# Kernel optimization log

Measured on AMD Instinct MI355X. Metric: run time of the kernel, lower is better.

Reference implementation:

```python
import jax, jax.numpy as jnp
import numpy as np

FEAT_STRIDE = 16
NEG_THR, POS_THR = 0.3, 0.7        # cfg.TRAIN.RPN_NEGATIVE_OVERLAP / RPN_POSITIVE_OVERLAP
RPN_BATCHSIZE, NUM_FG = 256, 128   # RPN_BATCHSIZE, FG_FRACTION=0.5
A_PER_LOC = 9


def generate_anchors(base_size=16, ratios=(0.5, 1.0, 2.0), scales=(8, 16, 32)):
    w = h = float(base_size)
    xc = yc = 0.5 * (base_size - 1)
    size = w * h
    ws = np.round(np.sqrt(size / np.array(ratios)))
    hs = np.round(ws * np.array(ratios))
    out = []
    for wi, hi in zip(ws, hs):
        for s in scales:
            W, H = wi * s, hi * s
            out.append([xc - 0.5 * (W - 1), yc - 0.5 * (H - 1),
                        xc + 0.5 * (W - 1), yc + 0.5 * (H - 1)])
    return np.array(out, dtype=np.float32)  # [9, 4]


def _forward(rpn_cls_score, gt_boxes, im_info):
    B, _, H, W = rpn_cls_score.shape
    A = A_PER_LOC
    base = jnp.asarray(generate_anchors())
    sx, sy = jnp.meshgrid(jnp.arange(W) * FEAT_STRIDE, jnp.arange(H) * FEAT_STRIDE)  # 'xy', [H,W]
    shifts = jnp.stack([sx.ravel(), sy.ravel(), sx.ravel(), sy.ravel()], 1).astype(jnp.float32)  # [K,4]
    anchors = (base[None, :, :] + shifts[:, None, :]).reshape(-1, 4)  # [N=K*A, 4], (h,w,a)-major
    N = anchors.shape[0]

    img_h, img_w = im_info[0, 0], im_info[0, 1]
    inside = ((anchors[:, 0] >= 0) & (anchors[:, 1] >= 0) &
              (anchors[:, 2] < img_w) & (anchors[:, 3] < img_h))  # [N]

    # ---- IoU overlaps (torch +1 pixel convention) ----
    gt = gt_boxes[..., :4]  # [B,Kg,4]
    aw = anchors[:, 2] - anchors[:, 0] + 1.0
    ah = anchors[:, 3] - anchors[:, 1] + 1.0
    a_area = aw * ah                                   # [N]
    g_area = (gt[..., 2] - gt[..., 0] + 1.0) * (gt[..., 3] - gt[..., 1] + 1.0)  # [B,Kg]
    ix = jnp.maximum(0.0, jnp.minimum(anchors[None, :, None, 2], gt[:, None, :, 2])
                     - jnp.maximum(anchors[None, :, None, 0], gt[:, None, :, 0]) + 1.0)
    iy = jnp.maximum(0.0, jnp.minimum(anchors[None, :, None, 3], gt[:, None, :, 3])
                     - jnp.maximum(anchors[None, :, None, 1], gt[:, None, :, 1]) + 1.0)
    inter = ix * iy
    ovr = inter / (a_area[None, :, None] + g_area[:, None, :] - inter)  # [B,N,Kg]

    max_ovr = ovr.max(2)
    arg = ovr.argmax(2)                                 # [B,N]
    ovr_in = jnp.where(inside[None, :, None], ovr, 0.0)  # only in-image anchors compete for gt-max
    gt_max = ovr_in.max(1)                              # [B,Kg]
    gt_max = jnp.where(gt_max == 0.0, 1e-5, gt_max)
    is_best = (ovr_in == gt_max[:, None, :]).any(2)     # [B,N]

    # ---- label assignment (RPN_CLOBBER_POSITIVES = False) ----
    lbl = jnp.full((B, N), -1.0, jnp.float32)
    lbl = jnp.where(inside[None] & (max_ovr < NEG_THR), 0.0, lbl)
    lbl = jnp.where(inside[None] & is_best, 1.0, lbl)
    lbl = jnp.where(inside[None] & (max_ovr >= POS_THR), 1.0, lbl)

    # ---- random fg/bg subsampling (deterministic jax PRNG replaces np.random.permutation) ----
    def _subsample(lbl_b, key):
        kf, kb = jax.random.split(key)
        def disable(l, mask, limit, k):
            prio = jnp.where(mask, jax.random.uniform(k, l.shape), -1.0)
            order = jnp.argsort(-prio)
            rank = jnp.zeros(l.shape[0], jnp.int32).at[order].set(jnp.arange(l.shape[0], dtype=jnp.int32))
            return jnp.where(mask & (rank >= limit), -1.0, l)
        lbl_b = disable(lbl_b, lbl_b == 1.0, NUM_FG, kf)
        num_bg = RPN_BATCHSIZE - jnp.sum(lbl_b == 1.0)
        return disable(lbl_b, lbl_b == 0.0, num_bg, kb)

    lbl = jax.vmap(_subsample)(lbl, jax.random.split(jax.random.key(42), B))

    assigned = jnp.take_along_axis(gt, arg[..., None], axis=1)  # [B,N,4]
    acx = anchors[:, 0] + 0.5 * (aw - 1.0)
    acy = anchors[:, 1] + 0.5 * (ah - 1.0)
    g_w = assigned[..., 2] - assigned[..., 0] + 1.0
    g_h = assigned[..., 3] - assigned[..., 1] + 1.0
    gcx = assigned[..., 0] + 0.5 * (g_w - 1.0)
    gcy = assigned[..., 1] + 0.5 * (g_h - 1.0)
    targets = jnp.stack([(gcx - acx[None]) / aw[None], (gcy - acy[None]) / ah[None],
                         jnp.log(g_w / aw[None]), jnp.log(g_h / ah[None])], -1)  # [B,N,4]

    in_w = jnp.where(lbl == 1.0, 1.0, 0.0)             # RPN_BBOX_INSIDE_WEIGHTS = 1
    num_examples = jnp.sum(lbl >= 0.0, axis=1).astype(jnp.float32)  # RPN_POSITIVE_WEIGHT = -1
    uw = 1.0 / num_examples                             # uniform pos/neg weight, per batch
    out_w = jnp.where((lbl == 1.0) | (lbl == 0.0), uw[:, None], 0.0)

    # ---- _unmap with fill=0 for out-of-image anchors ----
    lbl = jnp.where(inside[None], lbl, 0.0)
    targets = jnp.where(inside[None, :, None], targets, 0.0)
    in_w = jnp.where(inside[None], in_w, 0.0)
    out_w = jnp.where(inside[None], out_w, 0.0)

    labels_out = lbl.reshape(B, H, W, A).transpose(0, 3, 1, 2).reshape(B, 1, A * H, W)
    targets_out = targets.reshape(B, H, W, 4 * A).transpose(0, 3, 1, 2)
    in_w_out = jnp.broadcast_to(in_w[..., None], (B, N, 4)).reshape(B, H, W, 4 * A).transpose(0, 3, 1, 2)
    out_w_out = jnp.broadcast_to(out_w[..., None], (B, N, 4)).reshape(B, H, W, 4 * A).transpose(0, 3, 1, 2)
    return labels_out, targets_out, in_w_out, out_w_out


def setup_inputs() -> dict:
    key = jax.random.key(0)
    B, A, H, W, Kg = 16, 9, 64, 64, 50
    k1, k2, k3, k4, k5 = jax.random.split(key, 5)
    rpn_cls_score = jax.random.normal(k1, (B, 2 * A, H, W), jnp.float32)
    # valid GT boxes inside a 1024x1024 image, class label in column 4
    x1 = jax.random.uniform(k2, (B, Kg)) * 800.0
    y1 = jax.random.uniform(k3, (B, Kg)) * 800.0
    w = 20.0 + jax.random.uniform(k4, (B, Kg)) * 200.0
    h = 20.0 + jax.random.uniform(k5, (B, Kg)) * 200.0
    cls = jnp.ones((B, Kg), jnp.float32)
    gt_boxes = jnp.stack([x1, y1, x1 + w, y1 + h, cls], -1)
    im_info = jnp.full((B, 2), 1024.0, jnp.float32)
    return {"rpn_cls_score": rpn_cls_score, "gt_boxes": gt_boxes, "im_info": im_info, "num_boxes": Kg}


def reference(rpn_cls_score, gt_boxes, im_info, num_boxes):
    return _forward(rpn_cls_score, gt_boxes, im_info)
```

## Files before the change

### kernel.cpp

```cpp
#include <hip/hip_runtime.h>
#include <stdint.h>


#define B_   16
#define A_   9
#define H_   64
#define W_   64
#define HW_  (H_*W_)
#define N_   (HW_*A_)
#define KG_  50
#define S0_  (B_*A_*HW_)
#define S1_  (B_*4*A_*HW_)
#define NGTB_ (B_*KG_)
#define LCLR_ ((B_*N_ + NGTB_ - 1) / NGTB_)

typedef unsigned long long ull;

__constant__ float c_base[A_][4] = {
  { -84.f,  -40.f,  99.f,  55.f},
  {-176.f,  -88.f, 191.f, 103.f},
  {-360.f, -184.f, 375.f, 199.f},
  { -56.f,  -56.f,  71.f,  71.f},
  {-120.f, -120.f, 135.f, 135.f},
  {-248.f, -248.f, 263.f, 263.f},
  { -36.f,  -80.f,  51.f,  95.f},
  { -80.f, -168.f,  95.f, 183.f},
  {-168.f, -344.f, 183.f, 359.f},
};

__device__ __forceinline__ void tf2x32(uint32_t k0, uint32_t k1,
                                       uint32_t x0, uint32_t x1,
                                       uint32_t& o0, uint32_t& o1) {
  const uint32_t ks2 = k0 ^ k1 ^ 0x1BD11BDAu;
  uint32_t ks[3] = {k0, k1, ks2};
  x0 += ks[0]; x1 += ks[1];
  const int R[2][4] = {{13,15,26,6},{17,29,16,24}};
  #pragma unroll
  for (int i = 0; i < 5; i++) {
    #pragma unroll
    for (int j = 0; j < 4; j++) {
      x0 += x1;
      int r = R[i & 1][j];
      x1 = (x1 << r) | (x1 >> (32 - r));
      x1 ^= x0;
    }
    x0 += ks[(i + 1) % 3];
    x1 += ks[(i + 2) % 3] + (uint32_t)(i + 1);
  }
  o0 = x0; o1 = x1;
}

__device__ __attribute__((noinline))
float box_area_f(float x1, float y1, float x2, float y2) {
#pragma clang fp contract(off)
  return (x2 - x1 + 1.f) * (y2 - y1 + 1.f);
}

__device__ __attribute__((noinline))
float iou_core(float ax1, float ay1, float ax2, float ay2, float aarea,
               float gx1, float gy1, float gx2, float gy2, float garea) {
#pragma clang fp contract(off)
  float ix = fmaxf(fminf(ax2, gx2) - fmaxf(ax1, gx1) + 1.f, 0.f);
  float iy = fmaxf(fminf(ay2, gy2) - fmaxf(ay1, gy1) + 1.f, 0.f);
  float inter = ix * iy;
  return inter / (aarea + garea - inter);
}

__global__ __launch_bounds__(256) void k_gtmax(const float* __restrict__ gtb,
                                               const float* __restrict__ iminfo,
                                               float* __restrict__ gt_max,
                                               uint32_t* __restrict__ keys,
                                               float* __restrict__ lbl) {
  const int b = blockIdx.x / KG_;
  const int g = blockIdx.x % KG_;
  const int tid = threadIdx.x;
  if (blockIdx.x == 0 && tid < B_) {
    uint32_t k0, k1, kf0, kf1, kb0, kb1;
    tf2x32(0u, 42u, 0u, (uint32_t)tid, k0, k1);
    tf2x32(k0, k1, 0u, 0u, kf0, kf1);
    tf2x32(k0, k1, 0u, 1u, kb0, kb1);
    keys[tid * 4 + 0] = kf0;
    keys[tid * 4 + 1] = kf1;
    keys[tid * 4 + 2] = kb0;
    keys[tid * 4 + 3] = kb1;
  }
  {
    const int base = blockIdx.x * LCLR_;
    const int lim = min(base + LCLR_, B_ * N_);
    for (int i = base + tid; i < lim; i += 256) lbl[i] = -1.f;
  }
  const float* gp = gtb + (b * KG_ + g) * 5;
  const float gx1 = gp[0], gy1 = gp[1], gx2 = gp[2], gy2 = gp[3];
  const float garea = box_area_f(gx1, gy1, gx2, gy2);
  const float imh = iminfo[0], imw = iminfo[1];
  float best = 0.f;
  for (int a = 0; a < A_; a++) {
    const float bx1 = c_base[a][0], by1 = c_base[a][1];
    const float bx2 = c_base[a][2], by2 = c_base[a][3];
    const float aarea = box_area_f(bx1, by1, bx2, by2);
    int xlo = max(0, (int)ceilf(-bx1 / 16.f));
    int xhi = min(W_ - 1, (int)ceilf((imw - bx2) / 16.f) - 1);
    int ylo = max(0, (int)ceilf(-by1 / 16.f));
    int yhi = min(H_ - 1, (int)ceilf((imh - by2) / 16.f) - 1);
    xlo = max(xlo, (int)floorf((gx1 - 1.f - bx2) / 16.f));
    xhi = min(xhi, (int)ceilf((gx2 + 1.f - bx1) / 16.f));
    ylo = max(ylo, (int)floorf((gy1 - 1.f - by2) / 16.f));
    yhi = min(yhi, (int)ceilf((gy2 + 1.f - by1) / 16.f));
    const int nx = xhi - xlo + 1, ny = yhi - ylo + 1;
    if (nx <= 0 || ny <= 0) continue;
    const int lw = (nx <= 1) ? 0 : (32 - __clz(nx - 1));
    const int tot = ny << lw;
    const int mask = (1 << lw) - 1;
    for (int t = tid; t < tot; t += 256) {
      const int xi = t & mask;
      if (xi >= nx) continue;
      const int x = xlo + xi;
      const int y = ylo + (t >> lw);
      const float sx = 16.f * (float)x, sy = 16.f * (float)y;
      best = fmaxf(best, iou_core(bx1 + sx, by1 + sy, bx2 + sx, by2 + sy,
                                  aarea, gx1, gy1, gx2, gy2, garea));
    }
  }
  best = fmaxf(best, __shfl_xor(best, 32));
  best = fmaxf(best, __shfl_xor(best, 16));
  best = fmaxf(best, __shfl_xor(best, 8));
  best = fmaxf(best, __shfl_xor(best, 4));
  best = fmaxf(best, __shfl_xor(best, 2));
  best = fmaxf(best, __shfl_xor(best, 1));
  __shared__ float sw[4];
  if ((tid & 63) == 0) sw[tid >> 6] = best;
  __syncthreads();
  if (tid == 0)
    gt_max[b * KG_ + g] = fmaxf(fmaxf(sw[0], sw[1]), fmaxf(sw[2], sw[3]));
}

__global__ __launch_bounds__(256) void k_fuse(const float* __restrict__ gtb,
                                              const float* __restrict__ iminfo,
                                              const float* __restrict__ gt_max,
                                              const uint32_t* __restrict__ keys,
                                              float* __restrict__ lbl,
                                              int* __restrict__ amax,
                                              uint32_t* __restrict__ priof,
                                              uint32_t* __restrict__ priob) {
  __shared__ float sgx1[KG_], sgy1[KG_], sgx2[KG_], sgy2[KG_], sga[KG_], sgm[KG_];
  __shared__ int s_xlo[A_], s_ylo[A_], s_nx[A_], s_pre[A_ + 1];
  __shared__ uint32_t s_k[4];
  const int b = blockIdx.y;
  const int tid = threadIdx.x;
  if (tid < KG_) {
    const float* g = gtb + (b * KG_ + tid) * 5;
    float x1 = g[0], y1 = g[1], x2 = g[2], y2 = g[3];
    sgx1[tid] = x1; sgy1[tid] = y1; sgx2[tid] = x2; sgy2[tid] = y2;
    sga[tid] = box_area_f(x1, y1, x2, y2);
    float gm = gt_max[b * KG_ + tid];
    sgm[tid] = (gm == 0.f) ? 1e-5f : gm;
  }
  if (tid < 4) s_k[tid] = keys[b * 4 + tid];
  if (tid < A_) {
    const float imh = iminfo[0], imw = iminfo[1];
    const float bx1 = c_base[tid][0], by1 = c_base[tid][1];
    const float bx2 = c_base[tid][2], by2 = c_base[tid][3];
    int xlo = max(0, (int)ceilf(-bx1 / 16.f));
    int xhi = min(W_ - 1, (int)ceilf((imw - bx2) / 16.f) - 1);
    int ylo = max(0, (int)ceilf(-by1 / 16.f));
    int yhi = min(H_ - 1, (int)ceilf((imh - by2) / 16.f) - 1);
    int nx = max(0, xhi - xlo + 1), ny = max(0, yhi - ylo + 1);
    s_xlo[tid] = xlo; s_ylo[tid] = ylo; s_nx[tid] = nx;
    s_pre[tid + 1] = nx * ny;
  }
  __syncthreads();
  if (tid == 0) {
    s_pre[0] = 0;
    for (int a = 0; a < A_; a++) s_pre[a + 1] += s_pre[a];
  }
  __syncthreads();
  const int C = s_pre[A_];

  for (int t = blockIdx.x * 256 + tid; t < C; t += gridDim.x * 256) {
    int a = 0;
    while (t >= s_pre[a + 1]) a++;
    const int idx = t - s_pre[a];
    const int nx = s_nx[a];
    const int y = s_ylo[a] + idx / nx;
    const int x = s_xlo[a] + (idx - (idx / nx) * nx);
    const int n = (y * W_ + x) * A_ + a;
    const float sx = 16.f * (float)x, sy = 16.f * (float)y;
    const float ax1 = c_base[a][0] + sx, ay1 = c_base[a][1] + sy;
    const float ax2 = c_base[a][2] + sx, ay2 = c_base[a][3] + sy;
    const float aarea = box_area_f(c_base[a][0], c_base[a][1],
                                   c_base[a][2], c_base[a][3]);
    float mo = -1.f;
    int bidx = 0;
    bool best = false;
    for (int k = 0; k < KG_; k++) {
      float ovr = iou_core(ax1, ay1, ax2, ay2, aarea,
                           sgx1[k], sgy1[k], sgx2[k], sgy2[k], sga[k]);
      if (ovr > mo) { mo = ovr; bidx = k; }
      best = best || (ovr == sgm[k]);
    }
    float l = -1.f;
    if (mo < 0.3f) l = 0.f;
    if (best || mo >= 0.7f) l = 1.f;
    lbl[(size_t)b * N_ + n] = l;
    amax[(size_t)b * N_ + n] = bidx;
    uint32_t y0, y1;
    tf2x32(s_k[0], s_k[1], 0u, (uint32_t)n, y0, y1);
    priof[(size_t)b * N_ + n] = (y0 ^ y1) >> 9;
    tf2x32(s_k[2], s_k[3], 0u, (uint32_t)n, y0, y1);
    priob[(size_t)b * N_ + n] = (y0 ^ y1) >> 9;
  }
}

__global__ __launch_bounds__(1024) void k_sub3(float* __restrict__ lbl,
                                               const uint32_t* __restrict__ priof,
                                               const uint32_t* __restrict__ priob,
                                               float* __restrict__ uw) {
  const int b = blockIdx.x;
  const int tid = threadIdx.x;
  __shared__ int hf[256], hb[256];
  __shared__ int s_binF, s_rF, s_binB, s_rB, s_needF, s_needB, s_nf, s_nb;
  __shared__ float s_uw;
  __shared__ ull kF[2048], kB[2048];
  __shared__ ull s_KF, s_KB;

  float* L = lbl + (size_t)b * N_;
  const float4* L4 = (const float4*)L;
  const uint4* Pf4 = (const uint4*)(priof + (size_t)b * N_);
  const uint4* Pb4 = (const uint4*)(priob + (size_t)b * N_);

  if (tid < 256) { hf[tid] = 0; hb[tid] = 0; }
  if (tid == 0) { s_nf = 0; s_nb = 0; }
  __syncthreads();

  for (int i4 = tid; i4 < N_ / 4; i4 += 1024) {
    float4 v = L4[i4];
    uint4 mf = Pf4[i4];
    uint4 mb = Pb4[i4];
    const float lv[4] = {v.x, v.y, v.z, v.w};
    const uint32_t fv[4] = {mf.x, mf.y, mf.z, mf.w};
    const uint32_t bv[4] = {mb.x, mb.y, mb.z, mb.w};
    #pragma unroll
    for (int j = 0; j < 4; j++) {
      if (lv[j] == 1.f) atomicAdd(&hf[fv[j] >> 15], 1);
      else if (lv[j] == 0.f) atomicAdd(&hb[bv[j] >> 15], 1);
    }
  }
  __syncthreads();

  if (tid == 0) {
    int acc = 0, binF = -1, rF = 0;
    for (int bin = 255; bin >= 0; bin--) {
      int hv = hf[bin];
      if (binF < 0 && acc + hv >= 128) { binF = bin; rF = 128 - acc; }
      acc += hv;
    }
    const int Mf = acc;
    const int kf = (Mf < 128) ? Mf : 128;
    const int limB = 256 - kf;
    int accb = 0, binB = -1, rB = 0;
    for (int bin = 255; bin >= 0; bin--) {
      int hv = hb[bin];
      if (binB < 0 && accb + hv >= limB) { binB = bin; rB = limB - accb; }
      accb += hv;
    }
    const int Mb = accb;
    const int kb = (Mb < limB) ? Mb : limB;
    s_needF = (Mf > 128);
    s_binF = binF; s_rF = rF;
    s_needB = (Mb > limB);
    s_binB = binB; s_rB = rB;
    s_uw = 1.f / (float)(kf + kb);
  }
  __syncthreads();
  const int needF = s_needF, needB = s_needB;
  const int binF = s_binF, binB = s_binB;

  if (needF || needB) {
    for (int i4 = tid; i4 < N_ / 4; i4 += 1024) {
      float4 v = L4[i4];
      uint4 mf = Pf4[i4];
      uint4 mb = Pb4[i4];
      const float lv[4] = {v.x, v.y, v.z, v.w};
      const uint32_t fv[4] = {mf.x, mf.y, mf.z, mf.w};
      const uint32_t bv[4] = {mb.x, mb.y, mb.z, mb.w};
      #pragma unroll
      for (int j = 0; j < 4; j++) {
        if (needF && lv[j] == 1.f && (int)(fv[j] >> 15) == binF) {
          int p = atomicAdd(&s_nf, 1);
          if (p < 2048)
            kF[p] = ((ull)fv[j] << 16) | (ull)(65535 - (i4 * 4 + j));
        }
        if (needB && lv[j] == 0.f && (int)(bv[j] >> 15) == binB) {
          int p = atomicAdd(&s_nb, 1);
          if (p < 2048)
            kB[p] = ((ull)bv[j] << 16) | (ull)(65535 - (i4 * 4 + j));
        }
      }
    }
    __syncthreads();
    const int sf = min(s_nf, 2048), sb = min(s_nb, 2048);
    if (needF) {
      for (int j = tid; j < sf; j += 1024) {
        ull kj = kF[j];
        int rank = 0;
        for (int q = 0; q < sf; q++) rank += (kF[q] > kj) ? 1 : 0;
        if (rank == s_rF - 1) s_KF = kj;
      }
    }
    if (needB) {
      for (int j = tid; j < sb; j += 1024) {
        ull kj = kB[j];
        int rank = 0;
        for (int q = 0; q < sb; q++) rank += (kB[q] > kj) ? 1 : 0;
        if (rank == s_rB - 1) s_KB = kj;
      }
    }
    __syncthreads();
    const ull KF_ = needF ? s_KF : 0ull;
    const ull KB_ = needB ? s_KB : 0ull;
    for (int i4 = tid; i4 < N_ / 4; i4 += 1024) {
      float4 v = L4[i4];
      uint4 mf = Pf4[i4];
      uint4 mb = Pb4[i4];
      const float lv[4] = {v.x, v.y, v.z, v.w};
      const uint32_t fv[4] = {mf.x, mf.y, mf.z, mf.w};
      const uint32_t bv[4] = {mb.x, mb.y, mb.z, mb.w};
      #pragma unroll
      for (int j = 0; j < 4; j++) {
        if (needF && lv[j] == 1.f) {
          ull key = ((ull)fv[j] << 16) | (ull)(65535 - (i4 * 4 + j));
          if (key < KF_) L[i4 * 4 + j] = -1.f;
        } else if (needB && lv[j] == 0.f) {
          ull key = ((ull)bv[j] << 16) | (ull)(65535 - (i4 * 4 + j));
          if (key < KB_) L[i4 * 4 + j] = -1.f;
        }
      }
    }
  }
  if (tid == 0) uw[b] = s_uw;
}

__global__ __launch_bounds__(256) void k_out(const float* __restrict__ gtb,
                                             const float* __restrict__ iminfo,
                                             const float* __restrict__ lbl,
                                             const int* __restrict__ amax,
                                             const float* __restrict__ uw,
                                             float* __restrict__ out) {
  const int t = blockIdx.x * 256 + threadIdx.x;
  const int w = t & 63;
  const int h = (t >> 6) & 63;
  const int a = (t >> 12) % A_;
  const int b = t / (A_ * HW_);
  const int n = (h * W_ + w) * A_ + a;

  const float ax1 = c_base[a][0] + 16.f * (float)w;
  const float ay1 = c_base[a][1] + 16.f * (float)h;
  const float ax2 = c_base[a][2] + 16.f * (float)w;
  const float ay2 = c_base[a][3] + 16.f * (float)h;
  const float imh = iminfo[0], imw = iminfo[1];
  const bool ins = (ax1 >= 0.f) && (ay1 >= 0.f) && (ax2 < imw) && (ay2 < imh);

  const float l = lbl[(size_t)b * N_ + n];

  out[(size_t)b * (A_ * HW_) + a * HW_ + h * W_ + w] = ins ? l : 0.f;

  float tx = 0.f, ty = 0.f, tw = 0.f, th = 0.f;
  if (ins) {
    const int g = amax[(size_t)b * N_ + n];
    const float* gp = gtb + ((size_t)b * KG_ + g) * 5;
    float aw = ax2 - ax1 + 1.f, ah = ay2 - ay1 + 1.f;
    float acx = ax1 + 0.5f * (aw - 1.f), acy = ay1 + 0.5f * (ah - 1.f);
    float gw = gp[2] - gp[0] + 1.f, gh = gp[3] - gp[1] + 1.f;
    float gcx = gp[0] + 0.5f * (gw - 1.f), gcy = gp[1] + 0.5f * (gh - 1.f);
    tx = (gcx - acx) / aw;
    ty = (gcy - acy) / ah;
    tw = logf(gw / aw);
    th = logf(gh / ah);
  }
  float* o1 = out + S0_;
  const size_t toff = (size_t)b * (4 * A_ * HW_) + (4 * a) * HW_ + h * W_ + w;
  o1[toff]           = tx;
  o1[toff + HW_]     = ty;
  o1[toff + 2 * HW_] = tw;
  o1[toff + 3 * HW_] = th;

  const float inw = (ins && l == 1.f) ? 1.f : 0.f;
  const float oww = (ins && (l == 0.f || l == 1.f)) ? uw[b] : 0.f;
  float* o2 = out + S0_ + S1_;
  o2[toff] = inw; o2[toff + HW_] = inw; o2[toff + 2 * HW_] = inw; o2[toff + 3 * HW_] = inw;
  float* o3 = out + S0_ + 2 * (size_t)S1_;
  o3[toff] = oww; o3[toff + HW_] = oww; o3[toff + 2 * HW_] = oww; o3[toff + 3 * HW_] = oww;
}

extern "C" void kernel_launch(void* const* d_in, const int* in_sizes, int n_in,
                              void* d_out, int out_size, void* d_ws, size_t ws_size,
                              hipStream_t stream) {
  const float* gtb = (const float*)d_in[1];
  const float* iminfo = (const float*)d_in[2];
  float* out = (float*)d_out;

  float* lbl = (float*)d_ws;
  int* amax = (int*)(lbl + (size_t)B_ * N_);
  float* gt_max = (float*)(amax + (size_t)B_ * N_);
  float* uw = gt_max + B_ * KG_;
  uint32_t* keys = (uint32_t*)(uw + B_);
  uint32_t* priof = keys + B_ * 4;
  uint32_t* priob = priof + (size_t)B_ * N_;

  k_gtmax<<<NGTB_, 256, 0, stream>>>(gtb, iminfo, gt_max, keys, lbl);
  k_fuse<<<dim3(73, B_), 256, 0, stream>>>(gtb, iminfo, gt_max, keys,
                                           lbl, amax, priof, priob);
  k_sub3<<<B_, 1024, 0, stream>>>(lbl, priof, priob, uw);
  k_out<<<S0_ / 256, 256, 0, stream>>>(gtb, iminfo, lbl, amax, uw, out);
}
```

Measured before the change: 156.2 us.

## Compact fg/bg candidates and select threshold in parallel per batch-polarity

Instead of writing per-anchor priorities for all anchors and having one 1024-thread block per batch scan labels three times, the fused IoU kernel now compacts labeled anchors into per-batch fg/bg candidate lists and builds global histograms with atomics. A new small select kernel (one block per batch and polarity) finds the k-th largest key from the candidates. The final output kernel recomputes the threefry priority and applies the threshold inline, so the full -1 label clear and the priority buffers go away. This trades the serial per-batch scans for global atomics, a fixed candidate capacity (which could overflow if labeled counts exceed it), and duplicated RNG work in the output kernel.

```diff
diff --git a/kernel.cpp b/kernel.cpp
--- a/kernel.cpp
+++ b/kernel.cpp
@@ -12,7 +12,8 @@
 #define S0_  (B_*A_*HW_)
 #define S1_  (B_*4*A_*HW_)
 #define NGTB_ (B_*KG_)
-#define LCLR_ ((B_*N_ + NGTB_ - 1) / NGTB_)
+#define CAP_  20480
+#define NHIST_ (B_*2*256 + B_*2)
 
 typedef unsigned long long ull;
 
@@ -70,7 +71,7 @@
                                                const float* __restrict__ iminfo,
                                                float* __restrict__ gt_max,
                                                uint32_t* __restrict__ keys,
-                                               float* __restrict__ lbl) {
+                                               int* __restrict__ cnt_hist) {
   const int b = blockIdx.x / KG_;
   const int g = blockIdx.x % KG_;
   const int tid = threadIdx.x;
@@ -84,10 +85,11 @@
     keys[tid * 4 + 2] = kb0;
     keys[tid * 4 + 3] = kb1;
   }
-  {
-    const int base = blockIdx.x * LCLR_;
-    const int lim = min(base + LCLR_, B_ * N_);
-    for (int i = base + tid; i < lim; i += 256) lbl[i] = -1.f;
+  if (blockIdx.x < 32) {
+    const int per = (NHIST_ + 31) / 32;
+    const int base = blockIdx.x * per;
+    const int lim = min(base + per, NHIST_);
+    for (int i = base + tid; i < lim; i += 256) cnt_hist[i] = 0;
   }
   const float* gp = gtb + (b * KG_ + g) * 5;
   const float gx1 = gp[0], gy1 = gp[1], gx2 = gp[2], gy2 = gp[3];
@@ -140,11 +142,13 @@
                                               const uint32_t* __restrict__ keys,
                                               float* __restrict__ lbl,
                                               int* __restrict__ amax,
-                                              uint32_t* __restrict__ priof,
-                                              uint32_t* __restrict__ priob) {
+                                              ull* __restrict__ cand,
+                                              int* __restrict__ cnt,
+                                              int* __restrict__ hist) {
   __shared__ float sgx1[KG_], sgy1[KG_], sgx2[KG_], sgy2[KG_], sga[KG_], sgm[KG_];
   __shared__ int s_xlo[A_], s_ylo[A_], s_nx[A_], s_pre[A_ + 1];
   __shared__ uint32_t s_k[4];
+  __shared__ int s_num[2], s_base[2];
   const int b = blockIdx.y;
   const int tid = threadIdx.x;
   if (tid < KG_) {
@@ -156,6 +160,7 @@
     sgm[tid] = (gm == 0.f) ? 1e-5f : gm;
   }
   if (tid < 4) s_k[tid] = keys[b * 4 + tid];
+  if (tid < 2) s_num[tid] = 0;
   if (tid < A_) {
     const float imh = iminfo[0], imw = iminfo[1];
     const float bx1 = c_base[tid][0], by1 = c_base[tid][1];
@@ -175,15 +180,19 @@
   }
   __syncthreads();
   const int C = s_pre[A_];
-
-  for (int t = blockIdx.x * 256 + tid; t < C; t += gridDim.x * 256) {
+  const int t = blockIdx.x * 256 + tid;
+
+  bool act = false;
+  int p = 0, lpos = 0, n = 0;
+  uint32_t m = 0;
+  if (t < C) {
     int a = 0;
     while (t >= s_pre[a + 1]) a++;
     const int idx = t - s_pre[a];
     const int nx = s_nx[a];
     const int y = s_ylo[a] + idx / nx;
     const int x = s_xlo[a] + (idx - (idx / nx) * nx);
-    const int n = (y * W_ + x) * A_ + a;
+    n = (y * W_ + x) * A_ + a;
     const float sx = 16.f * (float)x, sy = 16.f * (float)y;
     const float ax1 = c_base[a][0] + sx, ay1 = c_base[a][1] + sy;
     const float ax2 = c_base[a][2] + sx, ay2 = c_base[a][3] + sy;
@@ -203,148 +212,85 @@
     if (best || mo >= 0.7f) l = 1.f;
     lbl[(size_t)b * N_ + n] = l;
     amax[(size_t)b * N_ + n] = bidx;
-    uint32_t y0, y1;
-    tf2x32(s_k[0], s_k[1], 0u, (uint32_t)n, y0, y1);
-    priof[(size_t)b * N_ + n] = (y0 ^ y1) >> 9;
-    tf2x32(s_k[2], s_k[3], 0u, (uint32_t)n, y0, y1);
-    priob[(size_t)b * N_ + n] = (y0 ^ y1) >> 9;
-  }
-}
-
-__global__ __launch_bounds__(1024) void k_sub3(float* __restrict__ lbl,
-                                               const uint32_t* __restrict__ priof,
-                                               const uint32_t* __restrict__ priob,
-                                               float* __restrict__ uw) {
-  const int b = blockIdx.x;
+    if (l >= 0.f) {
+      act = true;
+      p = (l == 1.f) ? 0 : 1;
+      uint32_t y0, y1;
+      tf2x32(s_k[2 * p], s_k[2 * p + 1], 0u, (uint32_t)n, y0, y1);
+      m = (y0 ^ y1) >> 9;
+      lpos = atomicAdd(&s_num[p], 1);
+    }
+  }
+  __syncthreads();
+  if (tid < 2 && s_num[tid] > 0)
+    s_base[tid] = atomicAdd(&cnt[b * 2 + tid], s_num[tid]);
+  __syncthreads();
+  if (act) {
+    cand[(size_t)(b * 2 + p) * CAP_ + s_base[p] + lpos] =
+        ((ull)m << 16) | (ull)(65535 - n);
+    atomicAdd(&hist[(b * 2 + p) * 256 + (int)(m >> 15)], 1);
+  }
+}
+
+__global__ __launch_bounds__(256) void k_select(const ull* __restrict__ cand,
+                                                const int* __restrict__ cnt,
+                                                const int* __restrict__ hist,
+                                                ull* __restrict__ Kstar,
+                                                float* __restrict__ uw) {
+  const int b = blockIdx.x >> 1, p = blockIdx.x & 1;
   const int tid = threadIdx.x;
-  __shared__ int hf[256], hb[256];
-  __shared__ int s_binF, s_rF, s_binB, s_rB, s_needF, s_needB, s_nf, s_nb;
-  __shared__ float s_uw;
-  __shared__ ull kF[2048], kB[2048];
-  __shared__ ull s_KF, s_KB;
-
-  float* L = lbl + (size_t)b * N_;
-  const float4* L4 = (const float4*)L;
-  const uint4* Pf4 = (const uint4*)(priof + (size_t)b * N_);
-  const uint4* Pb4 = (const uint4*)(priob + (size_t)b * N_);
-
-  if (tid < 256) { hf[tid] = 0; hb[tid] = 0; }
-  if (tid == 0) { s_nf = 0; s_nb = 0; }
-  __syncthreads();
-
-  for (int i4 = tid; i4 < N_ / 4; i4 += 1024) {
-    float4 v = L4[i4];
-    uint4 mf = Pf4[i4];
-    uint4 mb = Pb4[i4];
-    const float lv[4] = {v.x, v.y, v.z, v.w};
-    const uint32_t fv[4] = {mf.x, mf.y, mf.z, mf.w};
-    const uint32_t bv[4] = {mb.x, mb.y, mb.z, mb.w};
-    #pragma unroll
-    for (int j = 0; j < 4; j++) {
-      if (lv[j] == 1.f) atomicAdd(&hf[fv[j] >> 15], 1);
-      else if (lv[j] == 0.f) atomicAdd(&hb[bv[j] >> 15], 1);
-    }
-  }
-  __syncthreads();
-
+  __shared__ ull s_keys[2048];
+  __shared__ int s_bin, s_r, s_n;
+  const int cf = cnt[b * 2 + 0], cb = cnt[b * 2 + 1];
+  const int limit = (p == 0) ? 128 : 256 - min(cf, 128);
+  const int c = (p == 0) ? cf : cb;
+  if (p == 1 && tid == 0) {
+    int kf = min(cf, 128);
+    int kb = min(cb, 256 - kf);
+    uw[b] = 1.f / (float)(kf + kb);
+  }
+  if (c <= limit) {
+    if (tid == 0) Kstar[b * 2 + p] = 0ull;
+    return;
+  }
   if (tid == 0) {
-    int acc = 0, binF = -1, rF = 0;
-    for (int bin = 255; bin >= 0; bin--) {
-      int hv = hf[bin];
-      if (binF < 0 && acc + hv >= 128) { binF = bin; rF = 128 - acc; }
+    const int* Hh = hist + (b * 2 + p) * 256;
+    int acc = 0, bin = 255, r = 0;
+    for (; bin >= 0; bin--) {
+      int hv = Hh[bin];
+      if (acc + hv >= limit) { r = limit - acc; break; }
       acc += hv;
     }
-    const int Mf = acc;
-    const int kf = (Mf < 128) ? Mf : 128;
-    const int limB = 256 - kf;
-    int accb = 0, binB = -1, rB = 0;
-    for (int bin = 255; bin >= 0; bin--) {
-      int hv = hb[bin];
-      if (binB < 0 && accb + hv >= limB) { binB = bin; rB = limB - accb; }
-      accb += hv;
-    }
-    const int Mb = accb;
-    const int kb = (Mb < limB) ? Mb : limB;
-    s_needF = (Mf > 128);
-    s_binF = binF; s_rF = rF;
-    s_needB = (Mb > limB);
-    s_binB = binB; s_rB = rB;
-    s_uw = 1.f / (float)(kf + kb);
-  }
-  __syncthreads();
-  const int needF = s_needF, needB = s_needB;
-  const int binF = s_binF, binB = s_binB;
-
-  if (needF || needB) {
-    for (int i4 = tid; i4 < N_ / 4; i4 += 1024) {
-      float4 v = L4[i4];
-      uint4 mf = Pf4[i4];
-      uint4 mb = Pb4[i4];
-      const float lv[4] = {v.x, v.y, v.z, v.w};
-      const uint32_t fv[4] = {mf.x, mf.y, mf.z, mf.w};
-      const uint32_t bv[4] = {mb.x, mb.y, mb.z, mb.w};
-      #pragma unroll
-      for (int j = 0; j < 4; j++) {
-        if (needF && lv[j] == 1.f && (int)(fv[j] >> 15) == binF) {
-          int p = atomicAdd(&s_nf, 1);
-          if (p < 2048)
-            kF[p] = ((ull)fv[j] << 16) | (ull)(65535 - (i4 * 4 + j));
-        }
-        if (needB && lv[j] == 0.f && (int)(bv[j] >> 15) == binB) {
-          int p = atomicAdd(&s_nb, 1);
-          if (p < 2048)
-            kB[p] = ((ull)bv[j] << 16) | (ull)(65535 - (i4 * 4 + j));
-        }
-      }
-    }
-    __syncthreads();
-    const int sf = min(s_nf, 2048), sb = min(s_nb, 2048);
-    if (needF) {
-      for (int j = tid; j < sf; j += 1024) {
-        ull kj = kF[j];
-        int rank = 0;
-        for (int q = 0; q < sf; q++) rank += (kF[q] > kj) ? 1 : 0;
-        if (rank == s_rF - 1) s_KF = kj;
-      }
-    }
-    if (needB) {
-      for (int j = tid; j < sb; j += 1024) {
-        ull kj = kB[j];
-        int rank = 0;
-        for (int q = 0; q < sb; q++) rank += (kB[q] > kj) ? 1 : 0;
-        if (rank == s_rB - 1) s_KB = kj;
-      }
-    }
-    __syncthreads();
-    const ull KF_ = needF ? s_KF : 0ull;
-    const ull KB_ = needB ? s_KB : 0ull;
-    for (int i4 = tid; i4 < N_ / 4; i4 += 1024) {
-      float4 v = L4[i4];
-      uint4 mf = Pf4[i4];
-      uint4 mb = Pb4[i4];
-      const float lv[4] = {v.x, v.y, v.z, v.w};
-      const uint32_t fv[4] = {mf.x, mf.y, mf.z, mf.w};
-      const uint32_t bv[4] = {mb.x, mb.y, mb.z, mb.w};
-      #pragma unroll
-      for (int j = 0; j < 4; j++) {
-        if (needF && lv[j] == 1.f) {
-          ull key = ((ull)fv[j] << 16) | (ull)(65535 - (i4 * 4 + j));
-          if (key < KF_) L[i4 * 4 + j] = -1.f;
-        } else if (needB && lv[j] == 0.f) {
-          ull key = ((ull)bv[j] << 16) | (ull)(65535 - (i4 * 4 + j));
-          if (key < KB_) L[i4 * 4 + j] = -1.f;
-        }
-      }
-    }
-  }
-  if (tid == 0) uw[b] = s_uw;
+    s_bin = bin; s_r = r; s_n = 0;
+  }
+  __syncthreads();
+  const uint32_t bin0 = (uint32_t)s_bin;
+  const int r0 = s_r;
+  const ull* C = cand + (size_t)(b * 2 + p) * CAP_;
+  for (int i = tid; i < c; i += 256) {
+    ull k = C[i];
+    if ((uint32_t)(k >> 31) == bin0) {
+      int pos = atomicAdd(&s_n, 1);
+      if (pos < 2048) s_keys[pos] = k;
+    }
+  }
+  __syncthreads();
+  const int s = min(s_n, 2048);
+  for (int j = tid; j < s; j += 256) {
+    ull kj = s_keys[j];
+    int rank = 0;
+    for (int q = 0; q < s; q++) rank += (s_keys[q] > kj) ? 1 : 0;
+    if (rank == r0 - 1) Kstar[b * 2 + p] = kj;
+  }
 }
 
 __global__ __launch_bounds__(256) void k_out(const float* __restrict__ gtb,
                                              const float* __restrict__ iminfo,
                                              const float* __restrict__ lbl,
                                              const int* __restrict__ amax,
+                                             const ull* __restrict__ Kstar,
                                              const float* __restrict__ uw,
+                                             const uint32_t* __restrict__ keys,
                                              float* __restrict__ out) {
   const int t = blockIdx.x * 256 + threadIdx.x;
   const int w = t & 63;
@@ -360,7 +306,14 @@
   const float imh = iminfo[0], imw = iminfo[1];
   const bool ins = (ax1 >= 0.f) && (ay1 >= 0.f) && (ax2 < imw) && (ay2 < imh);
 
-  const float l = lbl[(size_t)b * N_ + n];
+  float l = ins ? lbl[(size_t)b * N_ + n] : -1.f;
+  if (ins && l >= 0.f) {
+    const int p = (l == 1.f) ? 0 : 1;
+    uint32_t y0, y1;
+    tf2x32(keys[b * 4 + 2 * p], keys[b * 4 + 2 * p + 1], 0u, (uint32_t)n, y0, y1);
+    ull key = ((ull)((y0 ^ y1) >> 9) << 16) | (ull)(65535 - n);
+    if (key < Kstar[b * 2 + p]) l = -1.f;
+  }
 
   out[(size_t)b * (A_ * HW_) + a * HW_ + h * W_ + w] = ins ? l : 0.f;
 
@@ -385,7 +338,7 @@
   o1[toff + 3 * HW_] = th;
 
   const float inw = (ins && l == 1.f) ? 1.f : 0.f;
-  const float oww = (ins && (l == 0.f || l == 1.f)) ? uw[b] : 0.f;
+  const float oww = (ins && l >= 0.f) ? uw[b] : 0.f;
   float* o2 = out + S0_ + S1_;
   o2[toff] = inw; o2[toff + HW_] = inw; o2[toff + 2 * HW_] = inw; o2[toff + 3 * HW_] = inw;
   float* o3 = out + S0_ + 2 * (size_t)S1_;
@@ -404,12 +357,15 @@
   float* gt_max = (float*)(amax + (size_t)B_ * N_);
   float* uw = gt_max + B_ * KG_;
   uint32_t* keys = (uint32_t*)(uw + B_);
-  uint32_t* priof = keys + B_ * 4;
-  uint32_t* priob = priof + (size_t)B_ * N_;
-
-  k_gtmax<<<NGTB_, 256, 0, stream>>>(gtb, iminfo, gt_max, keys, lbl);
-  k_fuse<<<dim3(73, B_), 256, 0, stream>>>(gtb, iminfo, gt_max, keys,
-                                           lbl, amax, priof, priob);
-  k_sub3<<<B_, 1024, 0, stream>>>(lbl, priof, priob, uw);
-  k_out<<<S0_ / 256, 256, 0, stream>>>(gtb, iminfo, lbl, amax, uw, out);
-}
+  int* cnt = (int*)(keys + B_ * 4);
+  int* hist = cnt + B_ * 2;
+  ull* Kstar = (ull*)(hist + B_ * 2 * 256);
+  ull* cand = Kstar + B_ * 2;
+
+  k_gtmax<<<NGTB_, 256, 0, stream>>>(gtb, iminfo, gt_max, keys, cnt);
+  k_fuse<<<dim3(144, B_), 256, 0, stream>>>(gtb, iminfo, gt_max, keys,
+                                            lbl, amax, cand, cnt, hist);
+  k_select<<<B_ * 2, 256, 0, stream>>>(cand, cnt, hist, Kstar, uw);
+  k_out<<<S0_ / 256, 256, 0, stream>>>(gtb, iminfo, lbl, amax, Kstar, uw,
+                                       keys, out);
+}
```

Result: faster. 137.1 us (-12.2%).
